# Optimization experiments

Hardware: AMD Instinct MI355X
Metric: run time of the kernel (lower is better)

The kernel has to match this reference:

```python
import jax, jax.numpy as jnp
import numpy as np

PATCH = 9
RAD = PATCH // 2  # 4


def _spatial_correlation(a, b):
    """SpatialCorrelationSampler(kernel_size=1, patch_size=9, stride=1,
    padding=0, dilation_patch=1).
    a, b: [B, C, H, W] -> out: [B, 9, 9, H, W]
    out[b, pi, pj, i, j] = sum_c a[b,c,i,j] * b_zeropad[b,c, i+pi-4, j+pj-4]
    Computed one shift at a time (81 small reductions) so we never
    materialize an 81x-unfolded copy of b.
    """
    B, C, H, W = a.shape
    bp = jnp.pad(b, ((0, 0), (0, 0), (RAD, RAD), (RAD, RAD)))
    rows = []
    for di in range(PATCH):
        cols = []
        for dj in range(PATCH):
            # shifted view of b, then channel-dot with a -> [B, H, W]
            cols.append(jnp.sum(a * bp[:, :, di:di + H, dj:dj + W], axis=1))
        rows.append(jnp.stack(cols, axis=1))  # [B, 9, H, W]
    return jnp.stack(rows, axis=1)  # [B, 9, 9, H, W]


def setup_inputs() -> dict:
    key = jax.random.key(0)
    shapes = [(8, 64, 112, 112), (8, 128, 56, 56), (8, 256, 28, 28), (8, 512, 14, 14)]
    keys = jax.random.split(key, 8)
    inp = {}
    for i, s in enumerate(shapes):
        inp[f"rgb{i}"] = jax.random.normal(keys[i], s, dtype=jnp.float32)
        inp[f"depth{i}"] = jax.random.normal(keys[4 + i], s, dtype=jnp.float32)
    return inp


def reference(rgb0, rgb1, rgb2, rgb3, depth0, depth1, depth2, depth3):
    rgbs = [rgb0, rgb1, rgb2, rgb3]
    depths = [depth0, depth1, depth2, depth3]
    corrs = []
    for i in range(4):
        corrs.insert(0, _spatial_correlation(rgbs[i], depths[i]))
    # reversed order: (corr3, corr2, corr1, corr0)
    return tuple(corrs)
```

## Files before the change

kernel.cpp:

```cpp
#include <hip/hip_runtime.h>
#include <hip/hip_bf16.h>

#define THREADS 256

#define OFF3 0
#define OFF2 127008
#define OFF1 635040
#define OFF0 2667168

#define N1 2032128
#define N2 508032
#define N3 127008
#define WS_L1 0
#define WS_L2 (2 * N1)
#define WS_L3 (WS_L2 + 4 * N2)
#define WS_FLOATS (WS_L3 + 16 * N3)
#define WS_BYTES ((size_t)WS_FLOATS * 4)

#define GB_L0 448
#define GB_L1 224
#define GB_L2 224
#define GB_L3 112
#define GB_TOT (GB_L0 + GB_L1 + GB_L2 + GB_L3)

#define SMEM_FLOATS 9216

typedef __attribute__((ext_vector_type(8))) short bf16x8;
typedef __attribute__((ext_vector_type(4))) float f32x4;

__device__ __attribute__((aligned(64))) const float g_zeropage[16] = {};

__global__ void __launch_bounds__(THREADS)
zero_region_kernel(float* __restrict__ p, int n) {
    int i = blockIdx.x * blockDim.x + threadIdx.x;
    int stride = gridDim.x * blockDim.x;
    for (; i < n; i += stride) p[i] = 0.f;
}

__device__ __forceinline__ void gload16(const float* g, float* l) {
    __builtin_amdgcn_global_load_lds(
        (const __attribute__((address_space(1))) void*)g,
        (__attribute__((address_space(3))) void*)l, 16, 0, 0);
}
__device__ __forceinline__ void gload4(const float* g, float* l) {
    __builtin_amdgcn_global_load_lds(
        (const __attribute__((address_space(1))) void*)g,
        (__attribute__((address_space(3))) void*)l, 4, 0, 0);
}

__device__ __forceinline__ short bf16s(float f) {
    __hip_bfloat16 h = __float2bfloat16(f);
    return *reinterpret_cast<short*>(&h);
}

template<int N> __device__ __forceinline__ void wait_vm_lgkm0() {
    static_assert(N >= 0 && N <= 8, "unsupported count");
    if constexpr (N == 0) asm volatile("s_waitcnt vmcnt(0) lgkmcnt(0)" ::: "memory");
    else if constexpr (N == 1) asm volatile("s_waitcnt vmcnt(1) lgkmcnt(0)" ::: "memory");
    else if constexpr (N == 2) asm volatile("s_waitcnt vmcnt(2) lgkmcnt(0)" ::: "memory");
    else if constexpr (N == 3) asm volatile("s_waitcnt vmcnt(3) lgkmcnt(0)" ::: "memory");
    else if constexpr (N == 4) asm volatile("s_waitcnt vmcnt(4) lgkmcnt(0)" ::: "memory");
    else if constexpr (N == 5) asm volatile("s_waitcnt vmcnt(5) lgkmcnt(0)" ::: "memory");
    else if constexpr (N == 6) asm volatile("s_waitcnt vmcnt(6) lgkmcnt(0)" ::: "memory");
    else if constexpr (N == 7) asm volatile("s_waitcnt vmcnt(7) lgkmcnt(0)" ::: "memory");
    else                       asm volatile("s_waitcnt vmcnt(8) lgkmcnt(0)" ::: "memory");
}

template<int C, int H, int W, int TI, int TW, int SJ, int STRIPS, int CHUNKS,
         int CB, int MODE>
__device__ __forceinline__ void corr_level(const float* __restrict__ a,
                                           const float* __restrict__ b,
                                           float* __restrict__ out,
                                           int blk, float* __restrict__ smem)
{
    constexpr int PER_I = 9 * STRIPS;
    constexpr int USED  = TI * PER_I;
    constexpr bool F4   = (W % 4 == 0) && (TW % 4 == 0) && (SJ % 4 == 0);
    constexpr int BWQ0  = (TW + 8 + 3) / 4 + 1;
    constexpr int BWQ   = (BWQ0 % 2 == 0) ? BWQ0 + 1 : BWQ0;
    constexpr int BW_   = F4 ? BWQ * 4 : (((TW + 8 + 1) / 2) * 2);
    constexpr bool F2   = !F4 && (SJ % 2 == 0) && (TW % 2 == 0);
    constexpr int BROWS = TI + 8;
    constexpr int CCH   = C / CHUNKS;
    constexpr int HT    = (H + TI - 1) / TI;
    constexpr int WT    = W / TW;
    constexpr int NOUT  = 8 * 81 * H * W;
    constexpr int HW    = H * W;
    constexpr int BPC   = BROWS * BW_;
    constexpr int APC   = TI * TW;
    constexpr int NG    = CCH / CB;

    constexpr int F4PR = BW_ / 4;
    constexpr int NBF4 = BROWS * F4PR;
    constexpr int TOT4 = CB * NBF4;
    constexpr int K4   = (TOT4 + THREADS - 1) / THREADS;
    constexpr int TOTS = CB * BPC;
    constexpr int KS   = (TOTS + THREADS - 1) / THREADS;
    constexpr int A4PR = TW / 4;
    constexpr int NAF4 = TI * A4PR;
    constexpr int ATOT4 = CB * NAF4;
    constexpr int KA4  = (ATOT4 + THREADS - 1) / THREADS;
    constexpr int ATOTS = CB * APC;
    constexpr int KAS  = (ATOTS + THREADS - 1) / THREADS;

    constexpr int A_OFF = F4 ? (K4 * THREADS * 4) : (KS * THREADS);
    constexpr int BUFSZ = F4 ? ((K4 + KA4) * THREADS * 4) : ((KS + KAS) * THREADS);
    constexpr int KTOT  = F4 ? (K4 + KA4) : (KS + KAS);

    static_assert(USED <= THREADS && SJ * STRIPS == TW && CCH % CB == 0, "geom");
    static_assert(NG >= 2 && 3 * BUFSZ <= SMEM_FLOATS, "pipeline/smem");

    const int ch = blk % CHUNKS;
    int t = blk / CHUNKS;
    const int jt = t % WT; t /= WT;
    const int it = t % HT;
    const int bb = t / HT;
    const int i0 = it * TI;
    const int jb = jt * TW;

    const int tid = threadIdx.x;
    const int ii  = tid / PER_I;
    const int rem = tid - ii * PER_I;
    const int pi  = rem / STRIPS;
    const int s   = rem - pi * STRIPS;
    const int j0  = s * SJ;
    const bool active = (tid < USED) && ((H % TI == 0) || (i0 + ii) < H);

    const int c0 = ch * CCH;
    const float* __restrict__ bp = b + (size_t)(bb * C + c0) * HW;
    const float* __restrict__ ap = a + (size_t)(bb * C + c0) * HW;
    const float* zp = g_zeropage;

    float acc[9][SJ];
    #pragma unroll
    for (int p = 0; p < 9; ++p)
        #pragma unroll
        for (int u = 0; u < SJ; ++u) acc[p][u] = 0.f;

    const int wbase = tid & ~63;

    auto stage = [&](int cg, float* buf) {
        const float* gb = bp + (size_t)(cg * CB) * HW;
        const float* ga = ap + (size_t)(cg * CB) * HW;
        if constexpr (F4) {
            #pragma unroll
            for (int k = 0; k < K4; ++k) {
                const int f = tid + k * THREADS;
                const int cb  = f / NBF4;
                const int f2  = f - cb * NBF4;
                const int row = f2 / F4PR;
                const int c4  = f2 - row * F4PR;
                const int r   = i0 + row - 4;
                const int jj  = jb + (c4 - 1) * 4;
                const bool ok = (f < TOT4) && ((unsigned)r < (unsigned)H)
                                && (jj >= 0) && (jj <= W - 4);
                const float* src = ok ? (gb + cb * HW + r * W + jj) : zp;
                gload16(src, buf + (size_t)(k * THREADS + wbase) * 4);
            }
            #pragma unroll
            for (int k = 0; k < KA4; ++k) {
                const int f = tid + k * THREADS;
                const int cb  = f / NAF4;
                const int f2  = f - cb * NAF4;
                const int row = f2 / A4PR;
                const int c4  = f2 - row * A4PR;
                const bool ok = (f < ATOT4) && ((H % TI == 0) || (i0 + row) < H);
                const float* src = ok ? (ga + cb * HW + (i0 + row) * W + jb + c4 * 4)
                                      : zp;
                gload16(src, buf + A_OFF + (size_t)(k * THREADS + wbase) * 4);
            }
        } else {
            #pragma unroll
            for (int k = 0; k < KS; ++k) {
                const int f = tid + k * THREADS;
                const int cb  = f / BPC;
                const int f2  = f - cb * BPC;
                const int row = f2 / BW_;
                const int col = f2 - row * BW_;
                const int r   = i0 + row - 4;
                const int jj  = jb + col - 4;
                const bool ok = (f < TOTS) && ((unsigned)r < (unsigned)H)
                                && ((unsigned)jj < (unsigned)W);
                const float* src = ok ? (gb + cb * HW + r * W + jj) : zp;
                gload4(src, buf + (k * THREADS + wbase));
            }
            #pragma unroll
            for (int k = 0; k < KAS; ++k) {
                const int f = tid + k * THREADS;
                const int cb  = f / APC;
                const int f2  = f - cb * APC;
                const int row = f2 / TW;
                const int col = f2 - row * TW;
                const bool ok = (f < ATOTS) && ((H % TI == 0) || (i0 + row) < H);
                const float* src = ok ? (ga + cb * HW + (i0 + row) * W + jb + col)
                                      : zp;
                gload4(src, buf + A_OFF + (k * THREADS + wbase));
            }
        }
    };
    auto compute = [&](const float* buf) {
        if (!active) return;
        #pragma unroll
        for (int cb = 0; cb < CB; ++cb) {
            float breg[SJ + 8];
            float areg[SJ];
            const float* bbase = &buf[cb * BPC + (ii + pi) * BW_ + j0];
            const float* abase = &buf[A_OFF + cb * APC + ii * TW + j0];
            if constexpr (F4) {
                #pragma unroll
                for (int k = 0; k < (SJ + 8) / 4; ++k) {
                    float4 v = *reinterpret_cast<const float4*>(&bbase[4 * k]);
                    breg[4*k+0] = v.x; breg[4*k+1] = v.y;
                    breg[4*k+2] = v.z; breg[4*k+3] = v.w;
                }
                #pragma unroll
                for (int u = 0; u < SJ / 4; ++u) {
                    float4 v = *reinterpret_cast<const float4*>(&abase[4 * u]);
                    areg[4*u+0] = v.x; areg[4*u+1] = v.y;
                    areg[4*u+2] = v.z; areg[4*u+3] = v.w;
                }
            } else if constexpr (F2) {
                #pragma unroll
                for (int k = 0; k < (SJ + 8) / 2; ++k) {
                    float2 v = *reinterpret_cast<const float2*>(&bbase[2 * k]);
                    breg[2*k+0] = v.x; breg[2*k+1] = v.y;
                }
                #pragma unroll
                for (int u = 0; u < SJ / 2; ++u) {
                    float2 v = *reinterpret_cast<const float2*>(&abase[2 * u]);
                    areg[2*u+0] = v.x; areg[2*u+1] = v.y;
                }
            } else {
                #pragma unroll
                for (int k = 0; k < SJ + 8; ++k) breg[k] = bbase[k];
                #pragma unroll
                for (int u = 0; u < SJ; ++u) areg[u] = abase[u];
            }
            #pragma unroll
            for (int pj = 0; pj < 9; ++pj)
                #pragma unroll
                for (int u = 0; u < SJ; ++u)
                    acc[pj][u] = fmaf(areg[u], breg[u + pj], acc[pj][u]);
        }
    };

    float* bufA = smem;
    float* bufB = smem + BUFSZ;
    float* bufC = smem + 2 * BUFSZ;

    stage(0, bufA);
    stage(1, bufB);
    for (int cg = 0; cg < NG; ++cg) {
        if (cg < NG - 1) wait_vm_lgkm0<KTOT>();
        else             wait_vm_lgkm0<0>();
        __builtin_amdgcn_s_barrier();
        __builtin_amdgcn_sched_barrier(0);
        if (cg + 2 < NG) stage(cg + 2, bufC);
        compute(bufA);
        float* tp = bufA; bufA = bufB; bufB = bufC; bufC = tp;
    }

    if (active) {
        const int i = i0 + ii;
        float* obase = out;
        if constexpr (MODE == 1) obase = out + (size_t)ch * NOUT;
        #pragma unroll
        for (int pj = 0; pj < 9; ++pj) {
            float* o = obase + ((size_t)((bb * 9 + pi) * 9 + pj) * H + i) * W + jb + j0;
            if constexpr (MODE == 2) {
                #pragma unroll
                for (int u = 0; u < SJ; ++u) atomicAdd(&o[u], acc[pj][u]);
            } else if constexpr (F4) {
                #pragma unroll
                for (int u = 0; u < SJ / 4; ++u) {
                    float4 v;
                    v.x = acc[pj][4*u+0]; v.y = acc[pj][4*u+1];
                    v.z = acc[pj][4*u+2]; v.w = acc[pj][4*u+3];
                    *reinterpret_cast<float4*>(&o[4 * u]) = v;
                }
            } else {
                #pragma unroll
                for (int u = 0; u < SJ; ++u) o[u] = acc[pj][u];
            }
        }
    }
}

__device__ __forceinline__ void corr_l3_mfma(const float* __restrict__ a,
                                             const float* __restrict__ b,
                                             float* __restrict__ out,
                                             int blk, float* __restrict__ smem)
{
    constexpr int C = 512, HW = 196, W = 14;
    const int bb = blk / 14, i = blk % 14;
    const int y0a = ((i - 4) * W) & ~3;
    const int x0a = (i * W) & ~3;
    const int off = i * W - x0a;
    const int tid = threadIdx.x;
    const int lane = tid & 63, wid = tid >> 6;

    float* bl = smem;
    float* al = smem + 32 * 144;
    const float* zp = g_zeropage;
    const float* ab = a + (size_t)bb * C * HW;
    const float* bbase = b + (size_t)bb * C * HW;

    const int nt0 = wid * 2;
    const int ntc = (wid == 3) ? 3 : 2;

    f32x4 accv[3];
    #pragma unroll
    for (int t = 0; t < 3; ++t) accv[t] = (f32x4){0.f, 0.f, 0.f, 0.f};

    const int kgrp = lane >> 4;
    const int mn   = lane & 15;

    for (int ks = 0; ks < 16; ++ks) {
        __syncthreads();
        const float* bp = bbase + (size_t)(ks * 32) * HW;
        #pragma unroll
        for (int it = 0; it < 5; ++it) {
            const int f = tid + it * 256;
            if (f < 1152) {
                const int c = f / 36, q = f - 36 * c;
                const int y = y0a + 4 * q;
                const float* src = (y >= 0 && y <= 192) ? (bp + c * HW + y) : zp;
                gload16(src, smem + (size_t)4 * f);
            }
        }
        if (tid < 160) {
            const int c = tid / 5, q = tid - 5 * c;
            const int x = x0a + 4 * q;
            const float* src = (x <= 192) ? (ab + (size_t)(ks * 32 + c) * HW + x)
                                          : zp;
            gload16(src, smem + (size_t)4 * 1152 + (size_t)4 * tid);
        }
        __syncthreads();

        bf16x8 afr;
        #pragma unroll
        for (int e = 0; e < 8; ++e)
            afr[e] = bf16s(al[(kgrp * 8 + e) * 20 + off + mn]);

        #pragma unroll
        for (int t = 0; t < 3; ++t) {
            if (t < ntc) {
                const int nt = nt0 + t;
                bf16x8 bfr;
                #pragma unroll
                for (int e = 0; e < 8; ++e)
                    bfr[e] = bf16s(bl[(kgrp * 8 + e) * 144 + nt * 16 + mn]);
                accv[t] = __builtin_amdgcn_mfma_f32_16x16x32_bf16(
                    afr, bfr, accv[t], 0, 0, 0);
            }
        }
    }

    const int mrow0 = (lane >> 4) * 4;
    #pragma unroll
    for (int t = 0; t < 3; ++t) {
        if (t < ntc) {
            const int nt = nt0 + t;
            const int y  = y0a + nt * 16 + mn;
            const int ys = y + 56;
            const int yq = ys / 14;
            const int yi = yq - 4;
            const int yj = ys - 14 * yq;
            #pragma unroll
            for (int r = 0; r < 4; ++r) {
                const int m = mrow0 + r;
                const int x = i * 14 + m;
                if (x < 196) {
                    const int xi = x / 14;
                    const int xj = x - 14 * xi;
                    const int pi = yi - xi + 4;
                    const int pj = yj - xj + 4;
                    if ((unsigned)pi < 9u && (unsigned)pj < 9u)
                        out[(size_t)((bb * 9 + pi) * 9 + pj) * HW + x] = accv[t][r];
                }
            }
        }
    }
}

template<int PMODE>
__global__ void __launch_bounds__(THREADS)
corr_fused(const float* __restrict__ a0, const float* __restrict__ b0,
           const float* __restrict__ a1, const float* __restrict__ b1,
           const float* __restrict__ a2, const float* __restrict__ b2,
           const float* __restrict__ a3, const float* __restrict__ b3,
           float* __restrict__ out, float* __restrict__ ws)
{
    __shared__ float smem[SMEM_FLOATS];
    const int bid = blockIdx.x;
    if (bid < GB_L0) {
        const int blk = (bid % 8) * (GB_L0 / 8) + bid / 8;
        corr_level<64, 112, 112, 4, 56, 8, 7, 1, 2, 0>(
            a0, b0, out + OFF0, blk, smem);
    } else if (bid < GB_L0 + GB_L1) {
        const int r = bid - GB_L0;
        const int blk = (r % 8) * (GB_L1 / 8) + r / 8;
        corr_level<128, 56, 56, 4, 56, 8, 7, 2, 2, PMODE>(
            a1, b1, PMODE == 1 ? ws + WS_L1 : out + OFF1, blk, smem);
    } else if (bid < GB_L0 + GB_L1 + GB_L2) {
        const int r = bid - (GB_L0 + GB_L1);
        const int blk = (r % 8) * (GB_L2 / 8) + r / 8;
        corr_level<256, 28, 28, 4, 28, 4, 7, 4, 2, PMODE>(
            a2, b2, PMODE == 1 ? ws + WS_L2 : out + OFF2, blk, smem);
    } else {
        const int r = bid - (GB_L0 + GB_L1 + GB_L2);
        const int blk = (r % 8) * (GB_L3 / 8) + r / 8;
        corr_l3_mfma(a3, b3, out + OFF3, blk, smem);
    }
}

__global__ void __launch_bounds__(THREADS)
reduce_all_kernel(const float* __restrict__ ws, float* __restrict__ out)
{
    const int blk = blockIdx.x;
    const float4* src; float4* dst; int n4, chunks, nb, base;
    if (blk < 128) { src = (const float4*)(ws + WS_L2); dst = (float4*)(out + OFF2);
                     n4 = N2 / 4; chunks = 4; nb = 128; base = 0; }
    else           { src = (const float4*)(ws + WS_L1); dst = (float4*)(out + OFF1);
                     n4 = N1 / 4; chunks = 2; nb = 288; base = 128; }
    for (int i = (blk - base) * THREADS + threadIdx.x; i < n4; i += nb * THREADS) {
        float4 sv = src[i];
        for (int k = 1; k < chunks; ++k) {
            float4 tv = src[(size_t)k * n4 + i];
            sv.x += tv.x; sv.y += tv.y; sv.z += tv.z; sv.w += tv.w;
        }
        dst[i] = sv;
    }
}

extern "C" void kernel_launch(void* const* d_in, const int* in_sizes, int n_in,
                              void* d_out, int out_size, void* d_ws, size_t ws_size,
                              hipStream_t stream) {
    const float* a0 = (const float*)d_in[0];
    const float* b0 = (const float*)d_in[1];
    const float* a1 = (const float*)d_in[2];
    const float* b1 = (const float*)d_in[3];
    const float* a2 = (const float*)d_in[4];
    const float* b2 = (const float*)d_in[5];
    const float* a3 = (const float*)d_in[6];
    const float* b3 = (const float*)d_in[7];
    float* out = (float*)d_out;
    float* ws  = (float*)d_ws;

    if (ws_size >= WS_BYTES) {
        hipLaunchKernelGGL((corr_fused<1>), dim3(GB_TOT), dim3(THREADS), 0, stream,
                           a0, b0, a1, b1, a2, b2, a3, b3, out, ws);
        hipLaunchKernelGGL(reduce_all_kernel, dim3(416), dim3(THREADS), 0, stream,
                           ws, out);
    } else {
        hipLaunchKernelGGL(zero_region_kernel, dim3(512), dim3(THREADS), 0, stream,
                           out + OFF2, OFF0 - OFF2);
        hipLaunchKernelGGL((corr_fused<2>), dim3(GB_TOT), dim3(THREADS), 0, stream,
                           a0, b0, a1, b1, a2, b2, a3, b3, out, ws);
    }
}
```

Before: 60.24 us.

## Compute level-2 correlation with bf16 MFMA tiles instead of split-K partials

Level 2 (256 channels, 28x28) now uses a dedicated MFMA path, like level 3. Each block takes one image row of 28 pixels against a 272-wide band of shifted positions, accumulates all 256 channels in bf16 16x16x32 MFMAs, and scatters the valid 9x9 window entries straight into the output. The level-2 workspace partials and their reduction pass go away, so the reduce kernel only handles level 1 and launches fewer blocks. The cost is bf16 rounding of fp32 inputs, extra shared memory, and many wasted MFMA columns outside the 9x9 window.

Result: no change. 60.64 us (+0.7%).

```diff
diff --git a/kernel.cpp b/kernel.cpp
--- a/kernel.cpp
+++ b/kernel.cpp
@@ -23,7 +23,7 @@
 #define GB_L3 112
 #define GB_TOT (GB_L0 + GB_L1 + GB_L2 + GB_L3)
 
-#define SMEM_FLOATS 9216
+#define SMEM_FLOATS 9728
 
 typedef __attribute__((ext_vector_type(8))) short bf16x8;
 typedef __attribute__((ext_vector_type(4))) float f32x4;
@@ -383,6 +383,103 @@
     }
 }
 
+__device__ __forceinline__ void corr_l2_mfma(const float* __restrict__ a,
+                                             const float* __restrict__ b,
+                                             float* __restrict__ out,
+                                             int blk, float* __restrict__ smem)
+{
+    constexpr int C = 256, HW = 784, W = 28;
+    const int bb = blk / 28, i = blk % 28;
+    const int x0 = i * 28;
+    const int y0 = x0 - 116;
+    const int tid = threadIdx.x;
+    const int lane = tid & 63, wid = tid >> 6;
+
+    float* bl = smem;
+    float* al = smem + 32 * 272;
+    const float* zp = g_zeropage;
+    const float* ab = a + (size_t)bb * C * HW;
+    const float* bbase = b + (size_t)bb * C * HW;
+
+    f32x4 accv[9];
+    #pragma unroll
+    for (int t = 0; t < 9; ++t) accv[t] = (f32x4){0.f, 0.f, 0.f, 0.f};
+
+    const int kgrp = lane >> 4;
+    const int mn   = lane & 15;
+
+    for (int ks = 0; ks < 8; ++ks) {
+        __syncthreads();
+        const float* bp = bbase + (size_t)(ks * 32) * HW;
+        #pragma unroll
+        for (int it = 0; it < 9; ++it) {
+            const int f = tid + it * 256;
+            if (f < 2176) {
+                const int c = f / 68, q = f - 68 * c;
+                const int y = y0 + 4 * q;
+                const float* src = (y >= 0 && y <= HW - 4) ? (bp + c * HW + y) : zp;
+                gload16(src, smem + (size_t)4 * f);
+            }
+        }
+        {
+            const int c = tid >> 3, q = tid & 7;
+            const int x = x0 + 4 * q;
+            const float* src = (x <= HW - 4) ? (ab + (size_t)(ks * 32 + c) * HW + x)
+                                             : zp;
+            gload16(src, smem + (size_t)4 * 2176 + (size_t)4 * tid);
+        }
+        __syncthreads();
+
+        bf16x8 afr[2];
+        #pragma unroll
+        for (int mt = 0; mt < 2; ++mt)
+            #pragma unroll
+            for (int e = 0; e < 8; ++e)
+                afr[mt][e] = bf16s(al[(kgrp * 8 + e) * 32 + mt * 16 + mn]);
+
+        #pragma unroll
+        for (int t = 0; t < 9; ++t) {
+            const int p = wid + 4 * t;
+            if (p < 34) {
+                const int mt = p & 1, nt = p >> 1;
+                bf16x8 bfr;
+                #pragma unroll
+                for (int e = 0; e < 8; ++e)
+                    bfr[e] = bf16s(bl[(kgrp * 8 + e) * 272 + nt * 16 + mn]);
+                accv[t] = __builtin_amdgcn_mfma_f32_16x16x32_bf16(
+                    afr[mt], bfr, accv[t], 0, 0, 0);
+            }
+        }
+    }
+
+    const int mrow0 = (lane >> 4) * 4;
+    #pragma unroll
+    for (int t = 0; t < 9; ++t) {
+        const int p = wid + 4 * t;
+        if (p < 34) {
+            const int mt = p & 1, nt = p >> 1;
+            const int y  = y0 + nt * 16 + mn;
+            const int ys = y + 224;
+            const int yq = ys / 28;
+            const int yi = yq - 8;
+            const int yj = ys - 28 * yq;
+            #pragma unroll
+            for (int r = 0; r < 4; ++r) {
+                const int m = mt * 16 + mrow0 + r;
+                const int x = x0 + m;
+                if (x < HW) {
+                    const int xi = x / 28;
+                    const int xj = x - 28 * xi;
+                    const int pi = yi - xi + 4;
+                    const int pj = yj - xj + 4;
+                    if ((unsigned)pi < 9u && (unsigned)pj < 9u)
+                        out[(size_t)((bb * 9 + pi) * 9 + pj) * HW + x] = accv[t][r];
+                }
+            }
+        }
+    }
+}
+
 template<int PMODE>
 __global__ void __launch_bounds__(THREADS)
 corr_fused(const float* __restrict__ a0, const float* __restrict__ b0,
@@ -405,8 +502,7 @@
     } else if (bid < GB_L0 + GB_L1 + GB_L2) {
         const int r = bid - (GB_L0 + GB_L1);
         const int blk = (r % 8) * (GB_L2 / 8) + r / 8;
-        corr_level<256, 28, 28, 4, 28, 4, 7, 4, 2, PMODE>(
-            a2, b2, PMODE == 1 ? ws + WS_L2 : out + OFF2, blk, smem);
+        corr_l2_mfma(a2, b2, out + OFF2, blk, smem);
     } else {
         const int r = bid - (GB_L0 + GB_L1 + GB_L2);
         const int blk = (r % 8) * (GB_L3 / 8) + r / 8;
@@ -417,18 +513,14 @@
 __global__ void __launch_bounds__(THREADS)
 reduce_all_kernel(const float* __restrict__ ws, float* __restrict__ out)
 {
-    const int blk = blockIdx.x;
-    const float4* src; float4* dst; int n4, chunks, nb, base;
-    if (blk < 128) { src = (const float4*)(ws + WS_L2); dst = (float4*)(out + OFF2);
-                     n4 = N2 / 4; chunks = 4; nb = 128; base = 0; }
-    else           { src = (const float4*)(ws + WS_L1); dst = (float4*)(out + OFF1);
-                     n4 = N1 / 4; chunks = 2; nb = 288; base = 128; }
-    for (int i = (blk - base) * THREADS + threadIdx.x; i < n4; i += nb * THREADS) {
+    const float4* src = (const float4*)(ws + WS_L1);
+    float4* dst = (float4*)(out + OFF1);
+    const int n4 = N1 / 4;
+    for (int i = blockIdx.x * THREADS + threadIdx.x; i < n4;
+         i += gridDim.x * THREADS) {
         float4 sv = src[i];
-        for (int k = 1; k < chunks; ++k) {
-            float4 tv = src[(size_t)k * n4 + i];
-            sv.x += tv.x; sv.y += tv.y; sv.z += tv.z; sv.w += tv.w;
-        }
+        float4 tv = src[(size_t)n4 + i];
+        sv.x += tv.x; sv.y += tv.y; sv.z += tv.z; sv.w += tv.w;
         dst[i] = sv;
     }
 }
@@ -450,11 +542,11 @@
     if (ws_size >= WS_BYTES) {
         hipLaunchKernelGGL((corr_fused<1>), dim3(GB_TOT), dim3(THREADS), 0, stream,
                            a0, b0, a1, b1, a2, b2, a3, b3, out, ws);
-        hipLaunchKernelGGL(reduce_all_kernel, dim3(416), dim3(THREADS), 0, stream,
+        hipLaunchKernelGGL(reduce_all_kernel, dim3(288), dim3(THREADS), 0, stream,
                            ws, out);
     } else {
         hipLaunchKernelGGL(zero_region_kernel, dim3(512), dim3(THREADS), 0, stream,
-                           out + OFF2, OFF0 - OFF2);
+                           out + OFF1, OFF0 - OFF1);
         hipLaunchKernelGGL((corr_fused<2>), dim3(GB_TOT), dim3(THREADS), 0, stream,
                            a0, b0, a1, b1, a2, b2, a3, b3, out, ws);
     }
```
